# Kernel tuning notes

Hardware: AMD Instinct MI355X
Metric: run time of the kernel (lower is better)

Reference implementation:

```python
import jax, jax.numpy as jnp
import numpy as np

N_NODES = 50000
N_EDGES = 1600000
N_INPUT = 256
HID = 32
OUT = N_INPUT // 2
EPS = 1e-12


def gcn_conv(x, edge_index, W, b):
    # Standard GCNConv: D^{-1/2} (A + I) D^{-1/2} X W + b
    N = x.shape[0]
    loop = jnp.arange(N)
    src = jnp.concatenate([edge_index[0], loop])
    dst = jnp.concatenate([edge_index[1], loop])
    deg = jax.ops.segment_sum(jnp.ones_like(src, dtype=x.dtype), dst, num_segments=N)
    dinv = jax.lax.rsqrt(jnp.maximum(deg, 1.0))  # deg >= 1 due to self-loops
    norm = dinv[src] * dinv[dst]                  # [E+N]
    h = x @ W                                     # [N, out]
    msg = h[src] * norm[:, None]                  # gather + scale
    out = jax.ops.segment_sum(msg, dst, num_segments=N)
    return out + b


def l2_normalize(z):
    n = jnp.linalg.norm(z, axis=1, keepdims=True)
    return z / jnp.maximum(n, EPS)


def setup_inputs() -> dict:
    key = jax.random.key(0)
    ks = jax.random.split(key, 9)
    x = jax.random.normal(ks[0], (N_NODES, N_INPUT), dtype=jnp.float32)
    ei_u = jax.random.randint(ks[1], (2, N_EDGES), 0, N_NODES)
    ei_u2 = jax.random.randint(ks[2], (2, N_EDGES), 0, N_NODES)
    s_in = 1.0 / np.sqrt(N_INPUT)
    s_hid = 1.0 / np.sqrt(HID)
    W_in = jax.random.normal(ks[3], (N_INPUT, HID), dtype=jnp.float32) * s_in
    b_in = jnp.zeros((HID,), dtype=jnp.float32)
    W_hid = jax.random.normal(ks[4], (HID, HID), dtype=jnp.float32) * s_hid
    b_hid = jnp.zeros((HID,), dtype=jnp.float32)
    W_out = jax.random.normal(ks[5], (HID, OUT), dtype=jnp.float32) * s_hid
    b_out = jnp.zeros((OUT,), dtype=jnp.float32)
    return {"x": x, "edge_index_u": ei_u, "edge_index_u2": ei_u2,
            "W_in": W_in, "b_in": b_in, "W_hid": W_hid, "b_hid": b_hid,
            "W_out": W_out, "b_out": b_out}


def reference(x, edge_index_u, edge_index_u2, W_in, b_in, W_hid, b_hid, W_out, b_out):
    # layer 1 on both views
    x1 = gcn_conv(x, edge_index_u, W_in, b_in)
    x2 = gcn_conv(x, edge_index_u2, W_in, b_in)
    sim = jnp.sum(l2_normalize(x1) * l2_normalize(x2), axis=1, keepdims=True)
    mian = x1 + x2 * sim
    sup = x2 + x1 * sim
    # layer 2
    x1 = gcn_conv(mian, edge_index_u, W_hid, b_hid)
    x2 = gcn_conv(sup, edge_index_u2, W_hid, b_hid)
    sim = jnp.sum(l2_normalize(x1) * l2_normalize(x2), axis=1, keepdims=True)
    mian = x1 + x2 * sim
    sup = x2 + x1 * sim
    # layer 3: note both branches use edge_index_u (as in source)
    x1 = gcn_conv(mian, edge_index_u, W_out, b_out)
    x2 = gcn_conv(sup, edge_index_u, W_out, b_out)
    return jnp.concatenate([x1, x2], axis=1)
```

## Files before the change

### kernel.cpp

```cpp
#include <hip/hip_runtime.h>
#include <hip/hip_bf16.h>

#define NN 50000
#define NE 1600000
#define NIN 256
#define HID 32
#define FOUT 128
#define OSTR 256
#define NSB ((NN + 255) / 256)
#define CHUNK 2048
#define NCH ((NE + CHUNK - 1) / CHUNK)

static constexpr float EPS = 1e-12f;

__device__ __forceinline__ float b2f(unsigned short s) {
    return __uint_as_float((unsigned)s << 16);
}
__device__ __forceinline__ unsigned short f2b(float f) {
    unsigned u = __float_as_uint(f);
    u += 0x7FFFu + ((u >> 16) & 1u);
    return (unsigned short)(u >> 16);
}
__device__ __forceinline__ unsigned pack2(float a, float b) {
    return (unsigned)f2b(a) | ((unsigned)f2b(b) << 16);
}

__global__ __launch_bounds__(256) void k_hist(const int* __restrict__ dstA,
                                              const int* __restrict__ dstB,
                                              unsigned* __restrict__ hcA,
                                              unsigned* __restrict__ hcB, int half) {
    __shared__ unsigned h[NSB];
    for (int i = threadIdx.x; i < NSB; i += 256) h[i] = 0u;
    __syncthreads();
    bool sec = blockIdx.x >= half;
    int c = sec ? blockIdx.x - half : blockIdx.x;
    const int* dst = sec ? dstB : dstA;
    unsigned* hc = sec ? hcB : hcA;
    int beg = c * CHUNK, end = min(beg + CHUNK, NE);
    for (int e = beg + (int)threadIdx.x; e < end; e += 256)
        atomicAdd(&h[dst[e] >> 8], 1u);
    __syncthreads();
    for (int i = threadIdx.x; i < NSB; i += 256) hc[(size_t)c * NSB + i] = h[i];
}

__global__ __launch_bounds__(256) void k_cscan(unsigned* __restrict__ hcA,
                                               unsigned* __restrict__ hcB,
                                               unsigned* __restrict__ totA,
                                               unsigned* __restrict__ totB, int half) {
    __shared__ unsigned tile[256];
    __shared__ unsigned carry;
    bool sec = blockIdx.x >= half;
    int sb = sec ? blockIdx.x - half : blockIdx.x;
    unsigned* hc = sec ? hcB : hcA;
    unsigned* tot = sec ? totB : totA;
    if (threadIdx.x == 0) carry = 0u;
    __syncthreads();
    for (int base = 0; base < NCH; base += 256) {
        int c = base + (int)threadIdx.x;
        unsigned v = (c < NCH) ? hc[(size_t)c * NSB + sb] : 0u;
        tile[threadIdx.x] = v;
        __syncthreads();
        for (int off = 1; off < 256; off <<= 1) {
            unsigned t = (threadIdx.x >= (unsigned)off) ? tile[threadIdx.x - off] : 0u;
            __syncthreads();
            tile[threadIdx.x] += t;
            __syncthreads();
        }
        if (c < NCH) hc[(size_t)c * NSB + sb] = carry + tile[threadIdx.x] - v;
        __syncthreads();
        if (threadIdx.x == 0) carry += tile[255];
        __syncthreads();
    }
    if (threadIdx.x == 0) tot[sb] = carry;
}

__global__ __launch_bounds__(256) void k_bscan(const unsigned* __restrict__ totA,
                                               const unsigned* __restrict__ totB,
                                               int* __restrict__ bbA, int* __restrict__ bbB) {
    __shared__ unsigned tile[256];
    const unsigned* tot = blockIdx.x ? totB : totA;
    int* bb = blockIdx.x ? bbB : bbA;
    unsigned v = (threadIdx.x < NSB) ? tot[threadIdx.x] : 0u;
    tile[threadIdx.x] = v;
    __syncthreads();
    for (int off = 1; off < 256; off <<= 1) {
        unsigned t = (threadIdx.x >= (unsigned)off) ? tile[threadIdx.x - off] : 0u;
        __syncthreads();
        tile[threadIdx.x] += t;
        __syncthreads();
    }
    if (threadIdx.x < NSB) bb[threadIdx.x] = (int)(tile[threadIdx.x] - v);
    if (threadIdx.x == 0) bb[NSB] = NE;
}

__global__ __launch_bounds__(256) void k_bin1(const int* __restrict__ srcA,
                                              const int* __restrict__ dstA,
                                              const unsigned* __restrict__ hcA,
                                              const int* __restrict__ bbA,
                                              int* __restrict__ tmpA,
                                              const int* __restrict__ srcB,
                                              const int* __restrict__ dstB,
                                              const unsigned* __restrict__ hcB,
                                              const int* __restrict__ bbB,
                                              int* __restrict__ tmpB, int half) {
    __shared__ unsigned hbase[NSB];
    __shared__ unsigned hcur[NSB];
    __shared__ unsigned hscan[NSB];
    __shared__ unsigned tile[256];
    __shared__ unsigned pay[CHUNK];
    __shared__ unsigned gpos[CHUNK];
    bool sec = blockIdx.x >= half;
    int c = sec ? blockIdx.x - half : blockIdx.x;
    const int* src = sec ? srcB : srcA;
    const int* dst = sec ? dstB : dstA;
    const unsigned* hc = sec ? hcB : hcA;
    const int* bb = sec ? bbB : bbA;
    int* tmp = sec ? tmpB : tmpA;
    for (int i = threadIdx.x; i < NSB; i += 256) {
        hbase[i] = (unsigned)bb[i] + hc[(size_t)c * NSB + i];
        hcur[i] = 0u;
    }
    __syncthreads();
    int beg = c * CHUNK;
    int len = min(CHUNK, NE - beg);
    int d[8], s[8];
#pragma unroll
    for (int j = 0; j < 8; ++j) {
        int idx = j * 256 + (int)threadIdx.x;
        if (idx < len) { d[j] = dst[beg + idx]; s[j] = src[beg + idx]; }
        else d[j] = -1;
    }
#pragma unroll
    for (int j = 0; j < 8; ++j)
        if (d[j] >= 0) atomicAdd(&hcur[d[j] >> 8], 1u);
    __syncthreads();
    unsigned v = (threadIdx.x < NSB) ? hcur[threadIdx.x] : 0u;
    tile[threadIdx.x] = v;
    __syncthreads();
    for (int off = 1; off < 256; off <<= 1) {
        unsigned t = (threadIdx.x >= (unsigned)off) ? tile[threadIdx.x - off] : 0u;
        __syncthreads();
        tile[threadIdx.x] += t;
        __syncthreads();
    }
    if (threadIdx.x < NSB) {
        unsigned excl = tile[threadIdx.x] - v;
        hscan[threadIdx.x] = excl;
        hcur[threadIdx.x] = excl;
    }
    __syncthreads();
#pragma unroll
    for (int j = 0; j < 8; ++j) {
        if (d[j] >= 0) {
            int sb = d[j] >> 8;
            unsigned p = atomicAdd(&hcur[sb], 1u);
            pay[p] = ((unsigned)(d[j] & 255) << 16) | (unsigned)s[j];
            gpos[p] = hbase[sb] + (p - hscan[sb]);
        }
    }
    __syncthreads();
    for (int i = threadIdx.x; i < len; i += 256)
        tmp[gpos[i]] = (int)pay[i];
}

__global__ __launch_bounds__(256) void k_bin2(const int* __restrict__ tmpA,
                                              const int* __restrict__ bbA,
                                              unsigned short* __restrict__ csrA,
                                              unsigned* __restrict__ degA,
                                              float* __restrict__ dinvA,
                                              int* __restrict__ rpA,
                                              const int* __restrict__ tmpB,
                                              const int* __restrict__ bbB,
                                              unsigned short* __restrict__ csrB,
                                              unsigned* __restrict__ degB,
                                              float* __restrict__ dinvB,
                                              int* __restrict__ rpB, int half) {
    __shared__ unsigned cnt[256];
    __shared__ unsigned scan[256];
    __shared__ unsigned curs[256];
    bool sec = blockIdx.x >= half;
    int sb = sec ? blockIdx.x - half : blockIdx.x;
    const int* tmp = sec ? tmpB : tmpA;
    const int* bb = sec ? bbB : bbA;
    unsigned short* csr = sec ? csrB : csrA;
    unsigned* deg = sec ? degB : degA;
    float* dinv = sec ? dinvB : dinvA;
    int* rp = sec ? rpB : rpA;
    int beg = bb[sb], end = bb[sb + 1];
    cnt[threadIdx.x] = 0u;
    __syncthreads();
    for (int e = beg + (int)threadIdx.x; e < end; e += 256)
        atomicAdd(&cnt[(tmp[e] >> 16) & 255], 1u);
    __syncthreads();
    unsigned v = cnt[threadIdx.x];
    scan[threadIdx.x] = v;
    __syncthreads();
    for (int off = 1; off < 256; off <<= 1) {
        unsigned t = (threadIdx.x >= (unsigned)off) ? scan[threadIdx.x - off] : 0u;
        __syncthreads();
        scan[threadIdx.x] += t;
        __syncthreads();
    }
    unsigned excl = scan[threadIdx.x] - v;
    int n = sb * 256 + (int)threadIdx.x;
    if (n < NN) {
        deg[n] = v;
        rp[n] = beg + (int)excl;
        dinv[n] = rsqrtf((float)(v + 1u));
    }
    curs[threadIdx.x] = (unsigned)beg + excl;
    __syncthreads();
    for (int e = beg + (int)threadIdx.x; e < end; e += 256) {
        int p = tmp[e];
        unsigned pos = atomicAdd(&curs[(p >> 16) & 255], 1u);
        csr[pos] = (unsigned short)(p & 0xFFFF);
    }
}

__global__ __launch_bounds__(256) void k_gemm_in(const float* __restrict__ x,
                                                 const float* __restrict__ W,
                                                 const float* __restrict__ dinvU,
                                                 const float* __restrict__ dinvV,
                                                 unsigned short* __restrict__ hU,
                                                 unsigned short* __restrict__ hV, int N) {
    __shared__ float part[4 * 64 * 33];
    int lane = threadIdx.x & 63;
    int wv = __builtin_amdgcn_readfirstlane((int)(threadIdx.x >> 6));
    int row = blockIdx.x * 64 + lane;
    float acc[32];
#pragma unroll
    for (int j = 0; j < 32; ++j) acc[j] = 0.f;
    if (row < N) {
        const float4* xr = reinterpret_cast<const float4*>(x + (size_t)row * NIN);
#pragma unroll 4
        for (int i = 0; i < 16; ++i) {
            int k4 = wv * 16 + i;
            float4 v = xr[k4];
            const float* Wk = W + k4 * 4 * HID;
#pragma unroll
            for (int j = 0; j < 32; ++j) {
                acc[j] = fmaf(v.x, Wk[j], acc[j]);
                acc[j] = fmaf(v.y, Wk[HID + j], acc[j]);
                acc[j] = fmaf(v.z, Wk[2 * HID + j], acc[j]);
                acc[j] = fmaf(v.w, Wk[3 * HID + j], acc[j]);
            }
        }
    }
    float* pw = part + (wv * 64 + lane) * 33;
#pragma unroll
    for (int j = 0; j < 32; ++j) pw[j] = acc[j];
    __syncthreads();
    int r = threadIdx.x >> 2;
    int c0 = (threadIdx.x & 3) * 8;
    int orow = blockIdx.x * 64 + r;
    if (orow >= N) return;
    float s[8];
#pragma unroll
    for (int i = 0; i < 8; ++i) {
        s[i] = part[(0 * 64 + r) * 33 + c0 + i]
             + part[(1 * 64 + r) * 33 + c0 + i]
             + part[(2 * 64 + r) * 33 + c0 + i]
             + part[(3 * 64 + r) * 33 + c0 + i];
    }
    float du = dinvU[orow], dw = dinvV[orow];
    uint4 wu, wvv;
    wu.x = pack2(s[0] * du, s[1] * du); wu.y = pack2(s[2] * du, s[3] * du);
    wu.z = pack2(s[4] * du, s[5] * du); wu.w = pack2(s[6] * du, s[7] * du);
    wvv.x = pack2(s[0] * dw, s[1] * dw); wvv.y = pack2(s[2] * dw, s[3] * dw);
    wvv.z = pack2(s[4] * dw, s[5] * dw); wvv.w = pack2(s[6] * dw, s[7] * dw);
    *reinterpret_cast<uint4*>(hU + (size_t)orow * HID + c0) = wu;
    *reinterpret_cast<uint4*>(hV + (size_t)orow * HID + c0) = wvv;
}

__device__ __forceinline__ void pull_sum(const unsigned short* __restrict__ t,
                                         const unsigned short* __restrict__ csr,
                                         const int* __restrict__ rowptr,
                                         const unsigned* __restrict__ deg,
                                         float* __restrict__ out, int blk, int tid) {
    int node = blk * 32 + tid / 8;
    int q = tid % 8;
    if (node >= NN) return;
    const ushort4* h4 = reinterpret_cast<const ushort4*>(t);
    int beg = rowptr[node];
    int end = beg + (int)deg[node];
    ushort4 sv = h4[(size_t)node * 8 + q];
    float4 acc0, acc1;
    acc0.x = b2f(sv.x); acc0.y = b2f(sv.y); acc0.z = b2f(sv.z); acc0.w = b2f(sv.w);
    acc1.x = 0.f; acc1.y = 0.f; acc1.z = 0.f; acc1.w = 0.f;
    int e = beg;
    for (; e + 8 <= end; e += 8) {
        int s0 = csr[e],     s1 = csr[e + 1], s2 = csr[e + 2], s3 = csr[e + 3];
        int s4 = csr[e + 4], s5 = csr[e + 5], s6 = csr[e + 6], s7 = csr[e + 7];
        ushort4 v0 = h4[(size_t)s0 * 8 + q];
        ushort4 v1 = h4[(size_t)s1 * 8 + q];
        ushort4 v2 = h4[(size_t)s2 * 8 + q];
        ushort4 v3 = h4[(size_t)s3 * 8 + q];
        ushort4 v4 = h4[(size_t)s4 * 8 + q];
        ushort4 v5 = h4[(size_t)s5 * 8 + q];
        ushort4 v6 = h4[(size_t)s6 * 8 + q];
        ushort4 v7 = h4[(size_t)s7 * 8 + q];
        acc0.x += (b2f(v0.x) + b2f(v1.x)) + (b2f(v2.x) + b2f(v3.x));
        acc0.y += (b2f(v0.y) + b2f(v1.y)) + (b2f(v2.y) + b2f(v3.y));
        acc0.z += (b2f(v0.z) + b2f(v1.z)) + (b2f(v2.z) + b2f(v3.z));
        acc0.w += (b2f(v0.w) + b2f(v1.w)) + (b2f(v2.w) + b2f(v3.w));
        acc1.x += (b2f(v4.x) + b2f(v5.x)) + (b2f(v6.x) + b2f(v7.x));
        acc1.y += (b2f(v4.y) + b2f(v5.y)) + (b2f(v6.y) + b2f(v7.y));
        acc1.z += (b2f(v4.z) + b2f(v5.z)) + (b2f(v6.z) + b2f(v7.z));
        acc1.w += (b2f(v4.w) + b2f(v5.w)) + (b2f(v6.w) + b2f(v7.w));
    }
    if (e + 4 <= end) {
        int s0 = csr[e], s1 = csr[e + 1], s2 = csr[e + 2], s3 = csr[e + 3];
        ushort4 v0 = h4[(size_t)s0 * 8 + q];
        ushort4 v1 = h4[(size_t)s1 * 8 + q];
        ushort4 v2 = h4[(size_t)s2 * 8 + q];
        ushort4 v3 = h4[(size_t)s3 * 8 + q];
        acc1.x += (b2f(v0.x) + b2f(v1.x)) + (b2f(v2.x) + b2f(v3.x));
        acc1.y += (b2f(v0.y) + b2f(v1.y)) + (b2f(v2.y) + b2f(v3.y));
        acc1.z += (b2f(v0.z) + b2f(v1.z)) + (b2f(v2.z) + b2f(v3.z));
        acc1.w += (b2f(v0.w) + b2f(v1.w)) + (b2f(v2.w) + b2f(v3.w));
        e += 4;
    }
    for (; e < end; ++e) {
        ushort4 v0 = h4[(size_t)csr[e] * 8 + q];
        acc0.x += b2f(v0.x); acc0.y += b2f(v0.y);
        acc0.z += b2f(v0.z); acc0.w += b2f(v0.w);
    }
    float4 acc;
    acc.x = acc0.x + acc1.x; acc.y = acc0.y + acc1.y;
    acc.z = acc0.z + acc1.z; acc.w = acc0.w + acc1.w;
    *reinterpret_cast<float4*>(out + (size_t)node * HID + q * 4) = acc;
}

__global__ __launch_bounds__(256) void k_pull_pair(
    const unsigned short* __restrict__ tA, const unsigned short* __restrict__ csrA,
    const int* __restrict__ rpA, const unsigned* __restrict__ degA, float* __restrict__ outA,
    const unsigned short* __restrict__ tB, const unsigned short* __restrict__ csrB,
    const int* __restrict__ rpB, const unsigned* __restrict__ degB, float* __restrict__ outB,
    int nblk) {
    int b = blockIdx.x;
    int xcd = b & 7;
    int blk = (b >> 3) * 4 + (xcd & 3);
    if (blk >= nblk) return;
    if (xcd >= 4) pull_sum(tB, csrB, rpB, degB, outB, blk, threadIdx.x);
    else          pull_sum(tA, csrA, rpA, degA, outA, blk, threadIdx.x);
}

__global__ __launch_bounds__(256) void k_mix1(const float* __restrict__ Su,
                                              const float* __restrict__ Sv,
                                              const float* __restrict__ dinvU,
                                              const float* __restrict__ dinvV,
                                              const float* __restrict__ bias,
                                              unsigned short* __restrict__ Tu,
                                              unsigned short* __restrict__ Tv) {
    int node = blockIdx.x * 32 + (threadIdx.x >> 3);
    int q = threadIdx.x & 7;
    if (node >= NN) return;
    float4 su = *reinterpret_cast<const float4*>(Su + (size_t)node * HID + 4 * q);
    float4 sv = *reinterpret_cast<const float4*>(Sv + (size_t)node * HID + 4 * q);
    float du = dinvU[node], dw = dinvV[node];
    float a0 = fmaf(su.x, du, bias[4 * q + 0]);
    float a1 = fmaf(su.y, du, bias[4 * q + 1]);
    float a2 = fmaf(su.z, du, bias[4 * q + 2]);
    float a3 = fmaf(su.w, du, bias[4 * q + 3]);
    float b0 = fmaf(sv.x, dw, bias[4 * q + 0]);
    float b1 = fmaf(sv.y, dw, bias[4 * q + 1]);
    float b2 = fmaf(sv.z, dw, bias[4 * q + 2]);
    float b3 = fmaf(sv.w, dw, bias[4 * q + 3]);
    float n1 = a0 * a0 + a1 * a1 + a2 * a2 + a3 * a3;
    float n2 = b0 * b0 + b1 * b1 + b2 * b2 + b3 * b3;
    float dt = a0 * b0 + a1 * b1 + a2 * b2 + a3 * b3;
#pragma unroll
    for (int m = 4; m >= 1; m >>= 1) {
        n1 += __shfl_xor(n1, m);
        n2 += __shfl_xor(n2, m);
        dt += __shfl_xor(dt, m);
    }
    float sim = dt / (fmaxf(sqrtf(n1), EPS) * fmaxf(sqrtf(n2), EPS));
    uint2 mu, mv;
    mu.x = pack2((a0 + b0 * sim) * du, (a1 + b1 * sim) * du);
    mu.y = pack2((a2 + b2 * sim) * du, (a3 + b3 * sim) * du);
    mv.x = pack2((b0 + a0 * sim) * dw, (b1 + a1 * sim) * dw);
    mv.y = pack2((b2 + a2 * sim) * dw, (b3 + a3 * sim) * dw);
    *reinterpret_cast<uint2*>(Tu + (size_t)node * HID + 4 * q) = mu;
    *reinterpret_cast<uint2*>(Tv + (size_t)node * HID + 4 * q) = mv;
}

__global__ __launch_bounds__(256) void k_hid_mix_pack(const float* __restrict__ Su,
                                                      const float* __restrict__ Sv,
                                                      const float* __restrict__ W,
                                                      const float* __restrict__ bias,
                                                      const float* __restrict__ dinvU,
                                                      const float* __restrict__ dinvV,
                                                      unsigned short* __restrict__ Pa,
                                                      unsigned short* __restrict__ Pb) {
    __shared__ float Ws[HID * HID];
    __shared__ float zu[32][33];
    __shared__ float zv[32][33];
    int t = threadIdx.x;
    for (int i = t; i < HID * HID; i += 256) Ws[i] = W[i];
    int nb = blockIdx.x * 32;
    int l = t >> 3, q = t & 7;
    int node = nb + l;
    {
        float4 fu = make_float4(0.f, 0.f, 0.f, 0.f), fv = fu;
        if (node < NN) {
            fu = *reinterpret_cast<const float4*>(Su + (size_t)node * HID + 4 * q);
            fv = *reinterpret_cast<const float4*>(Sv + (size_t)node * HID + 4 * q);
        }
        zu[l][4 * q + 0] = fu.x; zu[l][4 * q + 1] = fu.y;
        zu[l][4 * q + 2] = fu.z; zu[l][4 * q + 3] = fu.w;
        zv[l][4 * q + 0] = fv.x; zv[l][4 * q + 1] = fv.y;
        zv[l][4 * q + 2] = fv.z; zv[l][4 * q + 3] = fv.w;
    }
    __syncthreads();
    if (node >= NN) return;
    float a[4] = {0.f, 0.f, 0.f, 0.f};
    float b[4] = {0.f, 0.f, 0.f, 0.f};
#pragma unroll
    for (int k = 0; k < HID; ++k) {
        float zuk = zu[l][k], zvk = zv[l][k];
        const float* Wk = Ws + k * HID + 4 * q;
#pragma unroll
        for (int j = 0; j < 4; ++j) {
            a[j] = fmaf(zuk, Wk[j], a[j]);
            b[j] = fmaf(zvk, Wk[j], b[j]);
        }
    }
    float du = dinvU[node], dw = dinvV[node];
#pragma unroll
    for (int j = 0; j < 4; ++j) {
        a[j] = fmaf(a[j], du, bias[4 * q + j]);
        b[j] = fmaf(b[j], dw, bias[4 * q + j]);
    }
    float n1 = a[0]*a[0] + a[1]*a[1] + a[2]*a[2] + a[3]*a[3];
    float n2 = b[0]*b[0] + b[1]*b[1] + b[2]*b[2] + b[3]*b[3];
    float dt = a[0]*b[0] + a[1]*b[1] + a[2]*b[2] + a[3]*b[3];
#pragma unroll
    for (int m = 4; m >= 1; m >>= 1) {
        n1 += __shfl_xor(n1, m);
        n2 += __shfl_xor(n2, m);
        dt += __shfl_xor(dt, m);
    }
    float sim = dt / (fmaxf(sqrtf(n1), EPS) * fmaxf(sqrtf(n2), EPS));
    uint2 ma, mb;
    ma.x = pack2((a[0] + b[0] * sim) * du, (a[1] + b[1] * sim) * du);
    ma.y = pack2((a[2] + b[2] * sim) * du, (a[3] + b[3] * sim) * du);
    mb.x = pack2((b[0] + a[0] * sim) * du, (b[1] + a[1] * sim) * du);
    mb.y = pack2((b[2] + a[2] * sim) * du, (b[3] + a[3] * sim) * du);
    *reinterpret_cast<uint2*>(Pa + (size_t)node * HID + 4 * q) = ma;
    *reinterpret_cast<uint2*>(Pb + (size_t)node * HID + 4 * q) = mb;
}

__global__ __launch_bounds__(512) void k_gemm_out2(const float* __restrict__ Qa,
                                                   const float* __restrict__ Qb,
                                                   const float* __restrict__ dinvU,
                                                   const float* __restrict__ W,
                                                   const float* __restrict__ b,
                                                   float* __restrict__ out, int N) {
    int lane = threadIdx.x & 63;
    int wv = (int)(threadIdx.x >> 6);
    int view = __builtin_amdgcn_readfirstlane(wv >> 2);
    int c0 = __builtin_amdgcn_readfirstlane((wv & 3) * 32);
    int row = blockIdx.x * 64 + lane;
    if (row >= N) return;
    const float* Q = view ? Qb : Qa;
    const float4* q4 = reinterpret_cast<const float4*>(Q + (size_t)row * HID);
    float a[32];
#pragma unroll
    for (int j = 0; j < 32; ++j) a[j] = 0.f;
#pragma unroll 2
    for (int k4 = 0; k4 < 8; ++k4) {
        float4 v = q4[k4];
        const float* Wk = W + (k4 * 4) * FOUT + c0;
#pragma unroll
        for (int j = 0; j < 32; ++j) {
            a[j] = fmaf(v.x, Wk[j], a[j]);
            a[j] = fmaf(v.y, Wk[FOUT + j], a[j]);
            a[j] = fmaf(v.z, Wk[2 * FOUT + j], a[j]);
            a[j] = fmaf(v.w, Wk[3 * FOUT + j], a[j]);
        }
    }
    float du = dinvU[row];
    float* o = out + (size_t)row * OSTR + view * FOUT + c0;
#pragma unroll
    for (int g = 0; g < 8; ++g) {
        float4 r;
        r.x = fmaf(a[4*g+0], du, b[c0+4*g+0]);
        r.y = fmaf(a[4*g+1], du, b[c0+4*g+1]);
        r.z = fmaf(a[4*g+2], du, b[c0+4*g+2]);
        r.w = fmaf(a[4*g+3], du, b[c0+4*g+3]);
        *reinterpret_cast<float4*>(o + 4 * g) = r;
    }
}

extern "C" void kernel_launch(void* const* d_in, const int* in_sizes, int n_in,
                              void* d_out, int out_size, void* d_ws, size_t ws_size,
                              hipStream_t stream) {
    const float* x     = (const float*)d_in[0];
    const int*   ei_u  = (const int*)d_in[1];
    const int*   ei_u2 = (const int*)d_in[2];
    const float* W_in  = (const float*)d_in[3];
    const float* b_in  = (const float*)d_in[4];
    const float* W_hid = (const float*)d_in[5];
    const float* b_hid = (const float*)d_in[6];
    const float* W_out = (const float*)d_in[7];
    const float* b_out = (const float*)d_in[8];
    float* out = (float*)d_out;

    const int* src_u  = ei_u;
    const int* dst_u  = ei_u + NE;
    const int* src_u2 = ei_u2;
    const int* dst_u2 = ei_u2 + NE;

    char* w = (char*)d_ws;
    auto carve = [&](size_t bytes) {
        char* p = w;
        w += (bytes + 255) & ~(size_t)255;
        return p;
    };
    unsigned* hc_u   = (unsigned*)carve((size_t)NCH * NSB * sizeof(unsigned));
    unsigned* hc_u2  = (unsigned*)carve((size_t)NCH * NSB * sizeof(unsigned));
    unsigned* tot_u  = (unsigned*)carve(NSB * sizeof(unsigned));
    unsigned* tot_u2 = (unsigned*)carve(NSB * sizeof(unsigned));
    int*      bb_u   = (int*)carve((NSB + 1) * sizeof(int));
    int*      bb_u2  = (int*)carve((NSB + 1) * sizeof(int));
    unsigned* deg_u  = (unsigned*)carve(NN * sizeof(unsigned));
    unsigned* deg_u2 = (unsigned*)carve(NN * sizeof(unsigned));
    float*    dinv_u  = (float*)carve(NN * sizeof(float));
    float*    dinv_u2 = (float*)carve(NN * sizeof(float));
    int*      rp_u   = (int*)carve(NN * sizeof(int));
    int*      rp_u2  = (int*)carve(NN * sizeof(int));
    unsigned short* csr_u  = (unsigned short*)carve((size_t)NE * sizeof(unsigned short));
    unsigned short* csr_u2 = (unsigned short*)carve((size_t)NE * sizeof(unsigned short));
    unsigned short* hU = (unsigned short*)carve((size_t)NN * HID * sizeof(unsigned short));
    unsigned short* hV = (unsigned short*)carve((size_t)NN * HID * sizeof(unsigned short));
    unsigned short* Tu = (unsigned short*)carve((size_t)NN * HID * sizeof(unsigned short));
    unsigned short* Tv = (unsigned short*)carve((size_t)NN * HID * sizeof(unsigned short));
    unsigned short* Pa = (unsigned short*)carve((size_t)NN * HID * sizeof(unsigned short));
    unsigned short* Pb = (unsigned short*)carve((size_t)NN * HID * sizeof(unsigned short));
    float* Su = (float*)carve((size_t)NN * HID * sizeof(float));
    float* Sv = (float*)carve((size_t)NN * HID * sizeof(float));
    int* tmp_u  = (int*)Su;
    int* tmp_u2 = (int*)Sv;

    const int BLK = 256;
    const int gP32 = (NN + 31) / 32;
    const int nPair = ((gP32 + 3) / 4) * 8;
    const int gR64 = (NN + 63) / 64;

    k_hist<<<2 * NCH, BLK, 0, stream>>>(dst_u, dst_u2, hc_u, hc_u2, NCH);
    k_cscan<<<2 * NSB, BLK, 0, stream>>>(hc_u, hc_u2, tot_u, tot_u2, NSB);
    k_bscan<<<2, BLK, 0, stream>>>(tot_u, tot_u2, bb_u, bb_u2);
    k_bin1<<<2 * NCH, BLK, 0, stream>>>(src_u, dst_u, hc_u, bb_u, tmp_u,
                                        src_u2, dst_u2, hc_u2, bb_u2, tmp_u2, NCH);
    k_bin2<<<2 * NSB, BLK, 0, stream>>>(tmp_u, bb_u, csr_u, deg_u, dinv_u, rp_u,
                                        tmp_u2, bb_u2, csr_u2, deg_u2, dinv_u2, rp_u2, NSB);

    k_gemm_in<<<gR64, BLK, 0, stream>>>(x, W_in, dinv_u, dinv_u2, hU, hV, NN);
    k_pull_pair<<<nPair, BLK, 0, stream>>>(hU, csr_u, rp_u, deg_u, Su,
                                           hV, csr_u2, rp_u2, deg_u2, Sv, gP32);
    k_mix1<<<gP32, BLK, 0, stream>>>(Su, Sv, dinv_u, dinv_u2, b_in, Tu, Tv);

    k_pull_pair<<<nPair, BLK, 0, stream>>>(Tu, csr_u, rp_u, deg_u, Su,
                                           Tv, csr_u2, rp_u2, deg_u2, Sv, gP32);
    k_hid_mix_pack<<<gP32, BLK, 0, stream>>>(Su, Sv, W_hid, b_hid, dinv_u, dinv_u2, Pa, Pb);

    k_pull_pair<<<nPair, BLK, 0, stream>>>(Pa, csr_u, rp_u, deg_u, Su,
                                           Pb, csr_u, rp_u, deg_u, Sv, gP32);
    k_gemm_out2<<<gR64, 512, 0, stream>>>(Su, Sv, dinv_u, W_out, b_out, out, NN);

    (void)in_sizes; (void)n_in; (void)out_size; (void)ws_size;
}
```

Baseline: 205.9 us.

## Stage output GEMM tile in LDS for coalesced stores; double binning chunk size

The final output GEMM kernel now writes its results into a padded shared-memory tile, 32 rows at a time, then stores them to global memory with fully coalesced contiguous writes. Previously each lane wrote strided float4 segments of its own row. Separately, the edge-binning chunk grows from 2048 to 4096 edges per block, which halves the number of per-chunk histogram blocks at the cost of more registers per thread and less parallelism. The staging adds two barriers per half-tile and about 32KB of LDS per block, which may reduce occupancy.

```diff
diff --git a/kernel.cpp b/kernel.cpp
--- a/kernel.cpp
+++ b/kernel.cpp
@@ -8,7 +8,7 @@
 #define FOUT 128
 #define OSTR 256
 #define NSB ((NN + 255) / 256)
-#define CHUNK 2048
+#define CHUNK 4096
 #define NCH ((NE + CHUNK - 1) / CHUNK)
 
 static constexpr float EPS = 1e-12f;
@@ -123,15 +123,15 @@
     __syncthreads();
     int beg = c * CHUNK;
     int len = min(CHUNK, NE - beg);
-    int d[8], s[8];
-#pragma unroll
-    for (int j = 0; j < 8; ++j) {
+    int d[16], s[16];
+#pragma unroll
+    for (int j = 0; j < 16; ++j) {
         int idx = j * 256 + (int)threadIdx.x;
         if (idx < len) { d[j] = dst[beg + idx]; s[j] = src[beg + idx]; }
         else d[j] = -1;
     }
 #pragma unroll
-    for (int j = 0; j < 8; ++j)
+    for (int j = 0; j < 16; ++j)
         if (d[j] >= 0) atomicAdd(&hcur[d[j] >> 8], 1u);
     __syncthreads();
     unsigned v = (threadIdx.x < NSB) ? hcur[threadIdx.x] : 0u;
@@ -150,7 +150,7 @@
     }
     __syncthreads();
 #pragma unroll
-    for (int j = 0; j < 8; ++j) {
+    for (int j = 0; j < 16; ++j) {
         if (d[j] >= 0) {
             int sb = d[j] >> 8;
             unsigned p = atomicAdd(&hcur[sb], 1u);
@@ -457,39 +457,52 @@
                                                    const float* __restrict__ W,
                                                    const float* __restrict__ b,
                                                    float* __restrict__ out, int N) {
+    __shared__ float ob[32 * 257];
     int lane = threadIdx.x & 63;
     int wv = (int)(threadIdx.x >> 6);
     int view = __builtin_amdgcn_readfirstlane(wv >> 2);
     int c0 = __builtin_amdgcn_readfirstlane((wv & 3) * 32);
     int row = blockIdx.x * 64 + lane;
-    if (row >= N) return;
-    const float* Q = view ? Qb : Qa;
-    const float4* q4 = reinterpret_cast<const float4*>(Q + (size_t)row * HID);
+    bool active = row < N;
     float a[32];
 #pragma unroll
     for (int j = 0; j < 32; ++j) a[j] = 0.f;
+    if (active) {
+        const float* Q = view ? Qb : Qa;
+        const float4* q4 = reinterpret_cast<const float4*>(Q + (size_t)row * HID);
 #pragma unroll 2
-    for (int k4 = 0; k4 < 8; ++k4) {
-        float4 v = q4[k4];
-        const float* Wk = W + (k4 * 4) * FOUT + c0;
-#pragma unroll
-        for (int j = 0; j < 32; ++j) {
-            a[j] = fmaf(v.x, Wk[j], a[j]);
-            a[j] = fmaf(v.y, Wk[FOUT + j], a[j]);
-            a[j] = fmaf(v.z, Wk[2 * FOUT + j], a[j]);
-            a[j] = fmaf(v.w, Wk[3 * FOUT + j], a[j]);
-        }
-    }
-    float du = dinvU[row];
-    float* o = out + (size_t)row * OSTR + view * FOUT + c0;
-#pragma unroll
-    for (int g = 0; g < 8; ++g) {
-        float4 r;
-        r.x = fmaf(a[4*g+0], du, b[c0+4*g+0]);
-        r.y = fmaf(a[4*g+1], du, b[c0+4*g+1]);
-        r.z = fmaf(a[4*g+2], du, b[c0+4*g+2]);
-        r.w = fmaf(a[4*g+3], du, b[c0+4*g+3]);
-        *reinterpret_cast<float4*>(o + 4 * g) = r;
+        for (int k4 = 0; k4 < 8; ++k4) {
+            float4 v = q4[k4];
+            const float* Wk = W + (k4 * 4) * FOUT + c0;
+#pragma unroll
+            for (int j = 0; j < 32; ++j) {
+                a[j] = fmaf(v.x, Wk[j], a[j]);
+                a[j] = fmaf(v.y, Wk[FOUT + j], a[j]);
+                a[j] = fmaf(v.z, Wk[2 * FOUT + j], a[j]);
+                a[j] = fmaf(v.w, Wk[3 * FOUT + j], a[j]);
+            }
+        }
+    }
+    float du = active ? dinvU[row] : 0.f;
+    int r32 = lane & 31;
+    int hl = lane >> 5;
+    for (int p = 0; p < 2; ++p) {
+        if (hl == p) {
+            int off = r32 * 257 + view * FOUT + c0;
+#pragma unroll
+            for (int j = 0; j < 32; ++j)
+                ob[off + j] = fmaf(a[j], du, b[c0 + j]);
+        }
+        __syncthreads();
+        int rbase = blockIdx.x * 64 + p * 32;
+        int nrows = min(32, N - rbase);
+        if (nrows > 0) {
+            float* obase = out + (size_t)rbase * OSTR;
+            int total = nrows * OSTR;
+            for (int f = threadIdx.x; f < total; f += 512)
+                obase[f] = ob[f + (f >> 8)];
+        }
+        __syncthreads();
     }
 }
 
```

Result: faster. 198.2 us, median of 3 (-3.7%).
